# Performance work log

Measured on AMD Instinct MI355X. Metric: run time of the kernel, lower is better.

The kernel has to match this reference:

```python
import jax, jax.numpy as jnp
import numpy as np

N = 50000        # nodes
E = 800000       # edges (avg degree 16)
DIN = 256        # input feature dim
D = 128          # embedding_dim
B = 8            # graphs in batch
ITERS = 2        # num_iterations


def setup_inputs() -> dict:
    key = jax.random.key(0)
    ks = jax.random.split(key, 16)
    w = lambda k, shape: jax.random.normal(k, shape, jnp.float32) * 0.05
    z = lambda n: jnp.zeros((n,), jnp.float32)
    return {
        "nodes": jax.random.normal(ks[0], (N, DIN), jnp.float32),
        "edges": jax.random.randint(ks[1], (2, E), 0, N),
        "batch": jnp.sort(jax.random.randint(ks[2], (N,), 0, B)),
        # initial encoder Linear(DIN, D)
        "W_enc": w(ks[3], (DIN, D)), "b_enc": z(D),
        # parent aggregation MLP: Linear(2D, D) -> ReLU -> Linear(D, D)
        "Wp1": w(ks[4], (2 * D, D)), "bp1": z(D),
        "Wp2": w(ks[5], (D, D)), "bp2": z(D),
        # child aggregation MLP
        "Wc1": w(ks[6], (2 * D, D)), "bc1": z(D),
        "Wc2": w(ks[7], (D, D)), "bc2": z(D),
        # final agg: Linear(3D, 2D) -> ReLU -> Linear(2D, D)
        "Wf1": w(ks[8], (3 * D, 2 * D)), "bf1": z(2 * D),
        "Wf2": w(ks[9], (2 * D, D)), "bf2": z(D),
        # Conv1d(D, 2D, kernel=1) == Linear(D, 2D)
        "Wconv": w(ks[10], (D, 2 * D)), "bconv": z(2 * D),
    }


def _edge_agg(x, idx_i, idx_j, W1, b1, W2, b2, inv_deg):
    # message: mlp(cat(x_i, x_j)); scatter-sum at idx_i; degree-normalize.
    h = jnp.concatenate([x[idx_i], x[idx_j]], axis=1)         # [E, 2D]
    m = jax.nn.relu(h @ W1 + b1) @ W2 + b2                    # [E, D]
    agg = jax.ops.segment_sum(m, idx_i, num_segments=x.shape[0])
    return agg * inv_deg[:, None]


def reference(nodes, edges, batch, W_enc, b_enc, Wp1, bp1, Wp2, bp2,
              Wc1, bc1, Wc2, bc2, Wf1, bf1, Wf2, bf2, Wconv, bconv):
    src, dst = edges[0], edges[1]
    ones_e = jnp.ones((edges.shape[1],), nodes.dtype)
    deg_dst = jax.ops.segment_sum(ones_e, dst, num_segments=N)
    deg_src = jax.ops.segment_sum(ones_e, src, num_segments=N)
    inv_dst = jnp.where(deg_dst > 0, 1.0 / deg_dst, 0.0)
    inv_src = jnp.where(deg_src > 0, 1.0 / deg_src, 0.0)

    x = nodes @ W_enc + b_enc                                  # [N, D]
    for _ in range(ITERS):
        # Parent_Aggregation: x_i = x[dst], x_j = x[src], sum at dst, / in-deg
        fi = _edge_agg(x, dst, src, Wp1, bp1, Wp2, bp2, inv_dst)
        # Child_Aggregation:  x_i = x[src], x_j = x[dst], sum at src, / out-deg
        fo = _edge_agg(x, src, dst, Wc1, bc1, Wc2, bc2, inv_src)
        h = jnp.concatenate([x, fi, fo], axis=1)               # [N, 3D]
        x = x + (jax.nn.relu(h @ Wf1 + bf1) @ Wf2 + bf2)

    y = x @ Wconv + bconv                                      # conv1d k=1 -> [N, 2D]
    gmax = jax.ops.segment_max(y, batch, num_segments=B)       # global_max_pool
    cnt = jax.ops.segment_sum(jnp.ones((N,), y.dtype), batch, num_segments=B)
    gmean = jax.ops.segment_sum(y, batch, num_segments=B) / cnt[:, None]
    return jnp.concatenate([gmax, gmean], axis=1)              # [B, 4D]
```

## Files before the change

kernel.cpp:

```cpp
#include <hip/hip_runtime.h>
#include <hip/hip_bf16.h>
#include <float.h>

typedef __hip_bfloat16 bf16;
typedef short short8 __attribute__((ext_vector_type(8)));
typedef short short4v __attribute__((ext_vector_type(4)));
typedef float f32x4 __attribute__((ext_vector_type(4)));
typedef unsigned short u16;
typedef unsigned char u8;

__device__ __forceinline__ float toF(bf16 v) { return __bfloat162float(v); }
__device__ __forceinline__ float s2f(short s) {
    return __uint_as_float(((unsigned int)(unsigned short)s) << 16);
}
__device__ __forceinline__ short f2s(float f) {
    bf16 h = __float2bfloat16(f);
    return *(short*)&h;
}
__device__ __forceinline__ float rdw(const void* p, int i, int f) {
    return f ? toF(((const bf16*)p)[i]) : ((const float*)p)[i];
}

__global__ void diag_kernel(float* __restrict__ out, float v, int n) {
    int i = blockIdx.x * 256 + threadIdx.x;
    if (i < n) out[i] = v;
}

__global__ void init_kernel(int* __restrict__ deg2, float* __restrict__ cnt_gsum,
                            float* __restrict__ gmax, int* __restrict__ flag, int n2) {
    int i = blockIdx.x * 256 + threadIdx.x;
    if (i < n2) deg2[i] = 0;
    if (i < 8 + 2048) cnt_gsum[i] = 0.f;
    if (i < 2048) gmax[i] = -FLT_MAX;
    if (i == 0) *flag = 1;
}

__global__ void probe_kernel(const unsigned int* __restrict__ w, int nwords,
                             int* __restrict__ flag) {
    int i = blockIdx.x * 256 + threadIdx.x;
    bool bad = false;
    if (i < nwords) {
        float v = __uint_as_float((w[i] & 0xFFFFu) << 16);
        bad = !(v > -1e3f && v < 1e3f);
    }
    if (__any(bad) && (threadIdx.x & 63) == 0) atomicAnd(flag, 0);
}

struct M1 {
    const int* edges; int E;
    int* degd; int* degs; u8* rankd; u8* ranks;
    const int* batch; int Nn; float* cnt;
    const void* wsrc[7]; int woff[7]; bf16* wdst[7];
    int wK[7]; int wNC[7]; int wstart[8];
    const void* bsrc[8]; bf16* bdst[8]; int bn[8];
    const void* b1praw; const void* b1craw; bf16* b1wide;
    const int* flag;
    int sCnt, sSwz, sBias;
};

__global__ void mega1_kernel(M1 a) {
    int b = blockIdx.x, tid = threadIdx.x;
    if (b < a.sCnt) {
        const int* es = a.edges;
        const int* ed = a.edges + a.E;
        int e0 = (b * 256 + tid) * 4;
        if (e0 + 4 <= a.E) {
            int4 s4 = *(const int4*)(es + e0);
            int4 d4 = *(const int4*)(ed + e0);
            uchar4 rs, rd;
            rs.x = (u8)atomicAdd(&a.degs[s4.x], 1);
            rs.y = (u8)atomicAdd(&a.degs[s4.y], 1);
            rs.z = (u8)atomicAdd(&a.degs[s4.z], 1);
            rs.w = (u8)atomicAdd(&a.degs[s4.w], 1);
            rd.x = (u8)atomicAdd(&a.degd[d4.x], 1);
            rd.y = (u8)atomicAdd(&a.degd[d4.y], 1);
            rd.z = (u8)atomicAdd(&a.degd[d4.z], 1);
            rd.w = (u8)atomicAdd(&a.degd[d4.w], 1);
            *(uchar4*)(a.ranks + e0) = rs;
            *(uchar4*)(a.rankd + e0) = rd;
        } else {
            for (int e = e0; e < a.E; ++e) {
                a.ranks[e] = (u8)atomicAdd(&a.degs[es[e]], 1);
                a.rankd[e] = (u8)atomicAdd(&a.degd[ed[e]], 1);
            }
        }
    } else if (b < a.sSwz) {
        __shared__ float loc[8];
        if (tid < 8) loc[tid] = 0.f;
        __syncthreads();
        int i = (b - a.sCnt) * 256 + tid;
        if (i < a.Nn) atomicAdd(&loc[a.batch[i]], 1.0f);
        __syncthreads();
        if (tid < 8 && loc[tid] > 0.f) atomicAdd(&a.cnt[tid], loc[tid]);
    } else if (b < a.sBias) {
        int bb = b - a.sSwz;
        int seg = 0;
#pragma unroll
        for (int t = 1; t < 7; ++t) if (bb >= a.wstart[t]) seg = t;
        int i = (bb - a.wstart[seg]) * 256 + tid;
        int K = a.wK[seg], NC = a.wNC[seg];
        if (i < K * NC) {
            int KF = K >> 5;
            int j = i & 7;
            int ln = (i >> 3) & 63;
            int q = i >> 9;
            int kb = q % KF;
            int t = q / KF;
            int k = kb * 32 + (ln >> 4) * 8 + j;
            int n = t * 16 + (ln & 15);
            int idx = a.woff[seg] + k * NC + n;
            a.wdst[seg][i] = (*a.flag)
                ? ((const bf16*)a.wsrc[seg])[idx]
                : __float2bfloat16(((const float*)a.wsrc[seg])[idx]);
        }
    } else {
        int f = *a.flag;
#pragma unroll
        for (int t = 0; t < 8; ++t)
            for (int i = tid; i < a.bn[t]; i += 256)
                a.bdst[t][i] = f ? ((const bf16*)a.bsrc[t])[i]
                                 : __float2bfloat16(((const float*)a.bsrc[t])[i]);
        for (int i = tid; i < 512; i += 256) {
            float v = 0.f;
            if (i < 128) v = rdw(a.b1praw, i, f);
            else if (i >= 256 && i < 384) v = rdw(a.b1craw, i - 256, f);
            a.b1wide[i] = __float2bfloat16(v);
        }
    }
}

__device__ __forceinline__ void atomicMaxF(float* addr, float val) {
    unsigned int* ua = (unsigned int*)addr;
    unsigned int old = __float_as_uint(*addr);
    while (__uint_as_float(old) < val) {
        unsigned int assumed = old;
        old = atomicCAS(ua, assumed, __float_as_uint(val));
        if (old == assumed) break;
    }
}

template<int K, int NC> struct SB {
    static constexpr int APAD = K + 8;
    static constexpr int CPAD = NC + 8;
    static constexpr int AB = 64 * APAD * 2;
    static constexpr int CB = 64 * CPAD * 2;
    static constexpr int S = AB > CB ? AB : CB;
};

template<int K, int NC, int NSRC, int ADT, bool RELU, bool RES, bool POOL, bool STORE>
__device__ __forceinline__ void gemm_core(int bx,
    const bf16* A0, const bf16* A1, const bf16* A2,
    const bf16* WS, const bf16* bias, bf16* C, int M,
    const int* batch, float* gmax, float* gsum, char* smem) {
    constexpr int KF = K / 32;
    constexpr int NH = NC / 128;
    constexpr int APAD = SB<K, NC>::APAD;
    constexpr int CPAD = SB<K, NC>::CPAD;
    short* sA = (short*)smem;

    int tid = threadIdx.x;
    int m0blk = bx * 64;

    constexpr int C8 = K / 8;
    for (int idx = tid; idx < 64 * C8; idx += 256) {
        int r = idx / C8, c8 = idx % C8;
        int row = m0blk + r; row = row < M ? row : M - 1;
        const bf16* src;
        int off;
        if (NSRC == 1) { src = A0; off = c8 * 8; }
        else {
            int seg = c8 >> 4;
            src = seg == 0 ? A0 : (seg == 1 ? A1 : A2);
            off = (c8 & 15) * 8;
        }
        const size_t rs = (NSRC == 1) ? (size_t)K : (size_t)128;
        if (ADT == 0) {
            *(short8*)(sA + r * APAD + c8 * 8) =
                *(const short8*)((const short*)src + (size_t)row * rs + off);
        } else {
            const float* fp = (const float*)src;
            size_t base = (size_t)row * rs + off;
            float4 v0 = *(const float4*)(fp + base);
            float4 v1 = *(const float4*)(fp + base + 4);
            short8 o;
            o[0] = f2s(v0.x); o[1] = f2s(v0.y); o[2] = f2s(v0.z); o[3] = f2s(v0.w);
            o[4] = f2s(v1.x); o[5] = f2s(v1.y); o[6] = f2s(v1.z); o[7] = f2s(v1.w);
            *(short8*)(sA + r * APAD + c8 * 8) = o;
        }
    }
    __syncthreads();

    int wv = tid >> 6, ln = tid & 63;
    int quad = ln >> 4, ncol = ln & 15;
    int mw = wv * 16;

    short8 a[KF];
#pragma unroll
    for (int kb = 0; kb < KF; ++kb)
        a[kb] = *(const short8*)(sA + (mw + ncol) * APAD + kb * 32 + quad * 8);
    __syncthreads();

    short* sC = (short*)smem;
    const short8* wsp = (const short8*)WS;
#pragma unroll
    for (int h = 0; h < NH; ++h) {
        f32x4 acc[8];
#pragma unroll
        for (int t = 0; t < 8; ++t) acc[t] = (f32x4){0.f, 0.f, 0.f, 0.f};
        short8 bcur[8], bnxt[8];
#pragma unroll
        for (int t = 0; t < 8; ++t)
            bcur[t] = wsp[(size_t)((h * 8 + t) * KF) * 64 + ln];
#pragma unroll
        for (int kb = 0; kb < KF; ++kb) {
            if (kb + 1 < KF) {
#pragma unroll
                for (int t = 0; t < 8; ++t)
                    bnxt[t] = wsp[(size_t)((h * 8 + t) * KF + kb + 1) * 64 + ln];
            }
#pragma unroll
            for (int t = 0; t < 8; ++t)
                acc[t] = __builtin_amdgcn_mfma_f32_16x16x32_bf16(a[kb], bcur[t], acc[t], 0, 0, 0);
#pragma unroll
            for (int t = 0; t < 8; ++t) bcur[t] = bnxt[t];
        }
#pragma unroll
        for (int t = 0; t < 8; ++t) {
            float bv = bias ? toF(bias[h * 128 + t * 16 + ncol]) : 0.f;
#pragma unroll
            for (int r = 0; r < 4; ++r) {
                float v = acc[t][r] + bv;
                if (RELU) v = fmaxf(v, 0.f);
                sC[(mw + quad * 4 + r) * CPAD + h * 128 + t * 16 + ncol] = f2s(v);
            }
        }
    }
    __syncthreads();
    if (!STORE && !POOL) return;

    if (POOL) {
        int* bs = (int*)(smem + SB<K, NC>::S);
        if (tid < 64) {
            int row = m0blk + tid;
            bs[tid] = (row < M) ? batch[row] : -1;
        }
        __syncthreads();
        int cur_b = -1;
        float mx = -FLT_MAX, sm = 0.f;
        for (int r = 0; r < 64; ++r) {
            int b = bs[r];
            if (b < 0) break;
            float v = s2f(sC[r * CPAD + tid]);
            if (b != cur_b) {
                if (cur_b >= 0) {
                    atomicMaxF(&gmax[cur_b * 256 + tid], mx);
                    atomicAdd(&gsum[cur_b * 256 + tid], sm);
                }
                cur_b = b; mx = v; sm = v;
            } else {
                mx = fmaxf(mx, v);
                sm += v;
            }
        }
        if (cur_b >= 0) {
            atomicMaxF(&gmax[cur_b * 256 + tid], mx);
            atomicAdd(&gsum[cur_b * 256 + tid], sm);
        }
    } else {
        constexpr int OC8 = NC / 8;
        for (int idx = tid; idx < 64 * OC8; idx += 256) {
            int r = idx / OC8, c8 = idx % OC8;
            int row = m0blk + r;
            if (row < M) {
                short8 v = *(short8*)(sC + r * CPAD + c8 * 8);
                size_t o = (size_t)row * NC + c8 * 8;
                if (RES) {
                    short8 old = *(const short8*)((const short*)C + o);
#pragma unroll
                    for (int j = 0; j < 8; ++j) v[j] = f2s(s2f(v[j]) + s2f(old[j]));
                }
                *(short8*)((short*)C + o) = v;
            }
        }
    }
}

template<int K, int NC, int NSRC, bool RELU, bool RES, bool POOL>
__global__ __launch_bounds__(256, 2)
void gemm_mfma_kernel(const bf16* A0, const bf16* A1, const bf16* A2,
                      const bf16* WS, const bf16* bias, bf16* C, int M,
                      const int* batch, float* gmax, float* gsum) {
    __shared__ __align__(16) char smem[SB<K, NC>::S + (POOL ? 256 : 0)];
    gemm_core<K, NC, NSRC, 0, RELU, RES, POOL, true>(
        blockIdx.x, A0, A1, A2, WS, bias, C, M, batch, gmax, gsum, smem);
}

__global__ __launch_bounds__(256, 2)
void sei_kernel(const int* __restrict__ edges, int E,
                const u8* __restrict__ rankd, const u8* __restrict__ ranks,
                u16* __restrict__ adjd, u16* __restrict__ adjs, int CAP,
                const void* nodes_raw, const int* flag,
                const bf16* WSenc, const bf16* benc, bf16* x, int M,
                const int* degd, const int* degs,
                float* invd, float* invs,
                const void* w2praw, const void* w2craw, const void* wf1raw,
                const void* b2praw, const void* b2craw,
                bf16* wsf1, bf16* ub, bf16* vb,
                int gsc, int gb) {
    __shared__ __align__(16) char smem[SB<256, 128>::S];
    int b = blockIdx.x, tid = threadIdx.x;
    if (b < 384) {
        int i = b * 256 + tid;
        int j = i & 7;
        int ln2 = (i >> 3) & 63;
        int q = i >> 9;
        int kb = q % 12;
        int t = q / 12;
        int k = kb * 32 + (ln2 >> 4) * 8 + j;
        int n = t * 16 + (ln2 & 15);
        int f = *flag;
        float val;
        if (k < 128) {
            val = rdw(wf1raw, k * 256 + n, f);
        } else {
            const void* w2 = (k < 256) ? w2praw : w2craw;
            int arow = k & 127;
            int base = (k < 256) ? 128 : 256;
            float s = 0.f;
            for (int c = 0; c < 128; ++c)
                s += rdw(w2, arow * 128 + c, f) * rdw(wf1raw, (base + c) * 256 + n, f);
            val = s;
        }
        wsf1[i] = __float2bfloat16(val);
    } else if (b == 384) {
        if (tid < 256) {
            int f = *flag;
            float su = 0.f, sv = 0.f;
            for (int c = 0; c < 128; ++c) {
                su += rdw(b2praw, c, f) * rdw(wf1raw, (128 + c) * 256 + tid, f);
                sv += rdw(b2craw, c, f) * rdw(wf1raw, (256 + c) * 256 + tid, f);
            }
            ub[tid] = __float2bfloat16(su);
            vb[tid] = __float2bfloat16(sv);
        }
    } else if (b < 385 + gsc) {
        int e0 = ((b - 385) * 256 + tid) * 4;
        if (e0 + 4 <= E) {
            int4 s4 = *(const int4*)(edges + e0);
            int4 d4 = *(const int4*)(edges + E + e0);
            uchar4 rs = *(const uchar4*)(ranks + e0);
            uchar4 rd = *(const uchar4*)(rankd + e0);
            if (rs.x < CAP) adjs[s4.x * CAP + rs.x] = (u16)d4.x;
            if (rs.y < CAP) adjs[s4.y * CAP + rs.y] = (u16)d4.y;
            if (rs.z < CAP) adjs[s4.z * CAP + rs.z] = (u16)d4.z;
            if (rs.w < CAP) adjs[s4.w * CAP + rs.w] = (u16)d4.w;
            if (rd.x < CAP) adjd[d4.x * CAP + rd.x] = (u16)s4.x;
            if (rd.y < CAP) adjd[d4.y * CAP + rd.y] = (u16)s4.y;
            if (rd.z < CAP) adjd[d4.z * CAP + rd.z] = (u16)s4.z;
            if (rd.w < CAP) adjd[d4.w * CAP + rd.w] = (u16)s4.w;
        } else {
            for (int e = e0; e < E; ++e) {
                int s_ = edges[e], d_ = edges[E + e];
                if (ranks[e] < CAP) adjs[s_ * CAP + ranks[e]] = (u16)d_;
                if (rankd[e] < CAP) adjd[d_ * CAP + rankd[e]] = (u16)s_;
            }
        }
    } else if (b < 385 + gsc + gb) {
        int bx = b - 385 - gsc;
        if (*flag)
            gemm_core<256, 128, 1, 0, false, false, false, true>(
                bx, (const bf16*)nodes_raw, nullptr, nullptr, WSenc, benc, x, M,
                nullptr, nullptr, nullptr, smem);
        else
            gemm_core<256, 128, 1, 1, false, false, false, true>(
                bx, (const bf16*)nodes_raw, nullptr, nullptr, WSenc, benc, x, M,
                nullptr, nullptr, nullptr, smem);
    } else {
        int i = (b - 385 - gsc - gb) * 256 + tid;
        if (i < M) {
            int dd = degd[i]; invd[i] = dd > 0 ? 1.0f / (float)dd : 0.0f;
            int ds = degs[i]; invs[i] = ds > 0 ? 1.0f / (float)ds : 0.0f;
        }
    }
}

__device__ __forceinline__ void agg_body(int node, int tid,
        const int* __restrict__ deg, const u16* __restrict__ adj, int CAP,
        const float* __restrict__ inv,
        const short* __restrict__ PQ, int stride, bf16* __restrict__ S) {
    int ln = tid & 63;
    int g = ln >> 4, c8 = ln & 15;
    float p[8];
    {
        short8 pv = *(const short8*)(PQ + (size_t)node * stride + c8 * 8);
#pragma unroll
        for (int r = 0; r < 8; ++r) p[r] = s2f(pv[r]);
    }
    float a[8] = {0.f, 0.f, 0.f, 0.f, 0.f, 0.f, 0.f, 0.f};
    int d = deg[node]; d = d < CAP ? d : CAP;
    float invv = inv[node];
    const u16* ap = adj + (size_t)node * CAP;
    const short* Qb = PQ + 128 + c8 * 8;
    int k = g;
    for (; k + 28 < d; k += 32) {
        int j0 = ap[k],      j1 = ap[k + 4],  j2 = ap[k + 8],  j3 = ap[k + 12];
        int j4 = ap[k + 16], j5 = ap[k + 20], j6 = ap[k + 24], j7 = ap[k + 28];
        short8 q0 = *(const short8*)(Qb + (size_t)j0 * stride);
        short8 q1 = *(const short8*)(Qb + (size_t)j1 * stride);
        short8 q2 = *(const short8*)(Qb + (size_t)j2 * stride);
        short8 q3 = *(const short8*)(Qb + (size_t)j3 * stride);
        short8 q4 = *(const short8*)(Qb + (size_t)j4 * stride);
        short8 q5 = *(const short8*)(Qb + (size_t)j5 * stride);
        short8 q6 = *(const short8*)(Qb + (size_t)j6 * stride);
        short8 q7 = *(const short8*)(Qb + (size_t)j7 * stride);
#pragma unroll
        for (int r = 0; r < 8; ++r)
            a[r] += fmaxf(p[r] + s2f(q0[r]), 0.f) + fmaxf(p[r] + s2f(q1[r]), 0.f)
                  + fmaxf(p[r] + s2f(q2[r]), 0.f) + fmaxf(p[r] + s2f(q3[r]), 0.f)
                  + fmaxf(p[r] + s2f(q4[r]), 0.f) + fmaxf(p[r] + s2f(q5[r]), 0.f)
                  + fmaxf(p[r] + s2f(q6[r]), 0.f) + fmaxf(p[r] + s2f(q7[r]), 0.f);
    }
    for (; k + 12 < d; k += 16) {
        int j0 = ap[k], j1 = ap[k + 4], j2 = ap[k + 8], j3 = ap[k + 12];
        short8 q0 = *(const short8*)(Qb + (size_t)j0 * stride);
        short8 q1 = *(const short8*)(Qb + (size_t)j1 * stride);
        short8 q2 = *(const short8*)(Qb + (size_t)j2 * stride);
        short8 q3 = *(const short8*)(Qb + (size_t)j3 * stride);
#pragma unroll
        for (int r = 0; r < 8; ++r)
            a[r] += fmaxf(p[r] + s2f(q0[r]), 0.f) + fmaxf(p[r] + s2f(q1[r]), 0.f)
                  + fmaxf(p[r] + s2f(q2[r]), 0.f) + fmaxf(p[r] + s2f(q3[r]), 0.f);
    }
    for (; k < d; k += 4) {
        int j = ap[k];
        short8 q = *(const short8*)(Qb + (size_t)j * stride);
#pragma unroll
        for (int r = 0; r < 8; ++r) a[r] += fmaxf(p[r] + s2f(q[r]), 0.f);
    }
#pragma unroll
    for (int r = 0; r < 8; ++r) {
        a[r] += __shfl_xor(a[r], 16);
        a[r] += __shfl_xor(a[r], 32);
    }
    if (g == 0) {
        short8 o;
#pragma unroll
        for (int r = 0; r < 8; ++r) o[r] = f2s(a[r] * invv);
        *(short8*)((short*)S + (size_t)node * 128 + c8 * 8) = o;
    }
}

__global__ __launch_bounds__(256, 4)
void agg_kernel(const int* deg, const u16* adj, int CAP,
                const float* inv, const bf16* PQ, int stride,
                bf16* S, int M) {
    int node = blockIdx.x * 4 + (threadIdx.x >> 6);
    if (node >= M) return;
    agg_body(node, threadIdx.x, deg, adj, CAP, inv, (const short*)PQ, stride, S);
}

__global__ __launch_bounds__(256, 4)
void agg2_kernel(const int* degd, const u16* adjd, const float* invd,
                 const int* degs, const u16* adjs, const float* invs,
                 int CAP, const bf16* T, bf16* Sd, bf16* Ss, int M, int ga) {
    int b = blockIdx.x, wv = threadIdx.x >> 6;
    if (b < ga) {
        int node = b * 4 + wv;
        if (node < M)
            agg_body(node, threadIdx.x, degd, adjd, CAP, invd, (const short*)T, 512, Sd);
    } else {
        int node = (b - ga) * 4 + wv;
        if (node < M)
            agg_body(node, threadIdx.x, degs, adjs, CAP, invs, (const short*)T + 256, 512, Ss);
    }
}

template<bool FINAL>
__global__ __launch_bounds__(256, 2)
void mega_mlp_kernel(const bf16* __restrict__ x, const bf16* Sd, const bf16* Ss,
                     const int* __restrict__ degd, const int* __restrict__ degs,
                     const bf16* __restrict__ ub, const bf16* __restrict__ vb,
                     const bf16* WSf1, const bf16* bf1_,
                     const bf16* WSf2, const bf16* bf2_,
                     bf16* xio, int M,
                     const bf16* WSconv, const bf16* bconv,
                     const int* batch, float* gmax, float* gsum) {
    __shared__ __align__(16) char smem[52224 + 256];
    constexpr int RB = 17408;
    short* sm = (short*)smem;
    int tid = threadIdx.x;
    int m0blk = blockIdx.x * 64;

#pragma unroll
    for (int reg = 0; reg < 3; ++reg) {
        const short* sp = reg == 0 ? (const short*)x
                        : (reg == 1 ? (const short*)Sd : (const short*)Ss);
        for (int idx = tid; idx < 64 * 16; idx += 256) {
            int r = idx >> 4, c8 = idx & 15;
            int row = m0blk + r; row = row < M ? row : M - 1;
            *(short8*)(sm + reg * (RB / 2) + r * 136 + c8 * 8) =
                *(const short8*)(sp + (size_t)row * 128 + c8 * 8);
        }
    }
    __syncthreads();

    int wv = tid >> 6, ln = tid & 63;
    int quad = ln >> 4, ncol = ln & 15;
    int mw = wv * 16;

    short8 a1[12];
#pragma unroll
    for (int kb = 0; kb < 12; ++kb) {
        const short* sb = sm + (kb >> 2) * (RB / 2);
        a1[kb] = *(const short8*)(sb + (mw + ncol) * 136 + (kb & 3) * 32 + quad * 8);
    }
    __syncthreads();

    bool md[4], ms[4];
#pragma unroll
    for (int r = 0; r < 4; ++r) {
        int orow = m0blk + mw + quad * 4 + r; orow = orow < M ? orow : M - 1;
        md[r] = degd[orow] > 0;
        ms[r] = degs[orow] > 0;
    }

    short* sH = sm + RB / 2;
    const short8* w1 = (const short8*)WSf1;
#pragma unroll
    for (int h = 0; h < 2; ++h) {
        f32x4 acc[8];
#pragma unroll
        for (int t = 0; t < 8; ++t) acc[t] = (f32x4){0.f, 0.f, 0.f, 0.f};
        short8 bcur[8], bnxt[8];
#pragma unroll
        for (int t = 0; t < 8; ++t)
            bcur[t] = w1[(size_t)((h * 8 + t) * 12) * 64 + ln];
#pragma unroll
        for (int kb = 0; kb < 12; ++kb) {
            if (kb + 1 < 12) {
#pragma unroll
                for (int t = 0; t < 8; ++t)
                    bnxt[t] = w1[(size_t)((h * 8 + t) * 12 + kb + 1) * 64 + ln];
            }
#pragma unroll
            for (int t = 0; t < 8; ++t)
                acc[t] = __builtin_amdgcn_mfma_f32_16x16x32_bf16(a1[kb], bcur[t], acc[t], 0, 0, 0);
#pragma unroll
            for (int t = 0; t < 8; ++t) bcur[t] = bnxt[t];
        }
#pragma unroll
        for (int t = 0; t < 8; ++t) {
            int col = h * 128 + t * 16 + ncol;
            float bv = toF(bf1_[col]);
            float uu = toF(ub[col]);
            float vv = toF(vb[col]);
#pragma unroll
            for (int r = 0; r < 4; ++r) {
                float v = acc[t][r] + bv + (md[r] ? uu : 0.f) + (ms[r] ? vv : 0.f);
                sH[(mw + quad * 4 + r) * 264 + col] = f2s(fmaxf(v, 0.f));
            }
        }
    }
    __syncthreads();

    short8 a2[8];
#pragma unroll
    for (int kb = 0; kb < 8; ++kb)
        a2[kb] = *(const short8*)(sH + (mw + ncol) * 264 + kb * 32 + quad * 8);
    __syncthreads();

    f32x4 acc2[8];
#pragma unroll
    for (int t = 0; t < 8; ++t) acc2[t] = (f32x4){0.f, 0.f, 0.f, 0.f};
    const short8* w2 = (const short8*)WSf2;
    {
        short8 bcur[8], bnxt[8];
#pragma unroll
        for (int t = 0; t < 8; ++t) bcur[t] = w2[(size_t)(t * 8) * 64 + ln];
#pragma unroll
        for (int kb = 0; kb < 8; ++kb) {
            if (kb + 1 < 8) {
#pragma unroll
                for (int t = 0; t < 8; ++t)
                    bnxt[t] = w2[(size_t)(t * 8 + kb + 1) * 64 + ln];
            }
#pragma unroll
            for (int t = 0; t < 8; ++t)
                acc2[t] = __builtin_amdgcn_mfma_f32_16x16x32_bf16(a2[kb], bcur[t], acc2[t], 0, 0, 0);
#pragma unroll
            for (int t = 0; t < 8; ++t) bcur[t] = bnxt[t];
        }
    }
    short* sC2 = sm + RB / 2;
#pragma unroll
    for (int t = 0; t < 8; ++t) {
        float bv = toF(bf2_[t * 16 + ncol]);
#pragma unroll
        for (int r = 0; r < 4; ++r)
            sC2[(mw + quad * 4 + r) * 136 + t * 16 + ncol] = f2s(acc2[t][r] + bv);
    }
    __syncthreads();

    for (int idx = tid; idx < 64 * 16; idx += 256) {
        int r = idx >> 4, c8 = idx & 15;
        short8 v = *(short8*)(sC2 + r * 136 + c8 * 8);
        short8 old = *(const short8*)(sm + r * 136 + c8 * 8);
#pragma unroll
        for (int j = 0; j < 8; ++j) v[j] = f2s(s2f(v[j]) + s2f(old[j]));
        if (FINAL) {
            *(short8*)(sC2 + r * 136 + c8 * 8) = v;
        } else {
            int row = m0blk + r;
            if (row < M) *(short8*)((short*)xio + (size_t)row * 128 + c8 * 8) = v;
        }
    }
    if (!FINAL) return;
    __syncthreads();

    short8 a3[4];
#pragma unroll
    for (int kb = 0; kb < 4; ++kb)
        a3[kb] = *(const short8*)(sC2 + (mw + ncol) * 136 + kb * 32 + quad * 8);
    __syncthreads();

    short* sCc = sm;
    const short8* wc = (const short8*)WSconv;
#pragma unroll
    for (int h = 0; h < 2; ++h) {
        f32x4 acc[8];
#pragma unroll
        for (int t = 0; t < 8; ++t) acc[t] = (f32x4){0.f, 0.f, 0.f, 0.f};
        short8 bcur[8], bnxt[8];
#pragma unroll
        for (int t = 0; t < 8; ++t)
            bcur[t] = wc[(size_t)((h * 8 + t) * 4) * 64 + ln];
#pragma unroll
        for (int kb = 0; kb < 4; ++kb) {
            if (kb + 1 < 4) {
#pragma unroll
                for (int t = 0; t < 8; ++t)
                    bnxt[t] = wc[(size_t)((h * 8 + t) * 4 + kb + 1) * 64 + ln];
            }
#pragma unroll
            for (int t = 0; t < 8; ++t)
                acc[t] = __builtin_amdgcn_mfma_f32_16x16x32_bf16(a3[kb], bcur[t], acc[t], 0, 0, 0);
#pragma unroll
            for (int t = 0; t < 8; ++t) bcur[t] = bnxt[t];
        }
#pragma unroll
        for (int t = 0; t < 8; ++t) {
            float bv = toF(bconv[h * 128 + t * 16 + ncol]);
#pragma unroll
            for (int r = 0; r < 4; ++r)
                sCc[(mw + quad * 4 + r) * 264 + h * 128 + t * 16 + ncol] =
                    f2s(acc[t][r] + bv);
        }
    }
    __syncthreads();

    int* bs = (int*)(smem + 52224);
    if (tid < 64) {
        int row = m0blk + tid;
        bs[tid] = (row < M) ? batch[row] : -1;
    }
    __syncthreads();
    int cur_b = -1;
    float mx = -FLT_MAX, sum_ = 0.f;
    for (int r = 0; r < 64; ++r) {
        int b = bs[r];
        if (b < 0) break;
        float v = s2f(sCc[r * 264 + tid]);
        if (b != cur_b) {
            if (cur_b >= 0) {
                atomicMaxF(&gmax[cur_b * 256 + tid], mx);
                atomicAdd(&gsum[cur_b * 256 + tid], sum_);
            }
            cur_b = b; mx = v; sum_ = v;
        } else {
            mx = fmaxf(mx, v);
            sum_ += v;
        }
    }
    if (cur_b >= 0) {
        atomicMaxF(&gmax[cur_b * 256 + tid], mx);
        atomicAdd(&gsum[cur_b * 256 + tid], sum_);
    }
}

__global__ void out_kernel(const float* __restrict__ gmax, const float* __restrict__ gsum,
                           const float* __restrict__ cnt, const int* __restrict__ flag,
                           void* __restrict__ out) {
    int i = blockIdx.x * 256 + threadIdx.x;
    if (i < 8 * 512) {
        int b = i >> 9, c = i & 511;
        float v = (c < 256) ? gmax[b * 256 + c] : gsum[b * 256 + (c - 256)] / cnt[b];
        int f = *flag;
        if (!(v == v)) v = 1000.f + 100.f * (float)f;
        if (f) ((bf16*)out)[i] = __float2bfloat16(v);
        else   ((float*)out)[i] = v;
    }
}

extern "C" void kernel_launch(void* const* d_in, const int* in_sizes, int n_in,
                              void* d_out, int out_size, void* d_ws, size_t ws_size,
                              hipStream_t stream) {
    const int* edges = (const int*)d_in[1];
    const int* batch = (const int*)d_in[2];

    const int N_ = in_sizes[2];
    const int E_ = in_sizes[1] / 2;
    const size_t ND = (size_t)N_ * 128;

    char* p = (char*)d_ws;
    bf16* x  = (bf16*)p;      p += ND * 2;
    bf16* Sd = (bf16*)p;      p += ND * 2;
    bf16* Ss = (bf16*)p;      p += ND * 2;
    bf16* bias[8];
    for (int t = 0; t < 8; ++t) { bias[t] = (bf16*)p; p += 512 * 2; }
    bf16* ub      = (bf16*)p; p += 256 * 2;
    bf16* vb      = (bf16*)p; p += 256 * 2;
    bf16* b1wide  = (bf16*)p; p += 512 * 2;
    bf16* WSenc   = (bf16*)p; p += 256 * 128 * 2;
    bf16* WSpqall = (bf16*)p; p += 4 * 128 * 128 * 2;
    bf16* WSf1    = (bf16*)p; p += 384 * 256 * 2;
    bf16* WSf2    = (bf16*)p; p += 256 * 128 * 2;
    bf16* WSconv  = (bf16*)p; p += 128 * 256 * 2;
    int* degd    = (int*)p;   p += (size_t)N_ * 4;
    int* degs    = (int*)p;   p += (size_t)N_ * 4;
    float* invd  = (float*)p; p += (size_t)N_ * 4;
    float* invs  = (float*)p; p += (size_t)N_ * 4;
    float* cnt   = (float*)p; p += 8 * 4;
    float* gsum  = (float*)p; p += 2048 * 4;
    float* gmax  = (float*)p; p += 2048 * 4;
    int* flag    = (int*)p;   p += 64;
    u8* rankd    = (u8*)p;    p += ((size_t)E_ + 15) & ~(size_t)15;
    u8* ranks    = (u8*)p;    p += ((size_t)E_ + 15) & ~(size_t)15;

    size_t used = (size_t)(p - (char*)d_ws);
    size_t rem = ws_size > used ? ws_size - used : 0;
    int CAP = 0, wide = 0;
    if (N_ < 65536) {
        if      (rem >= (size_t)2 * N_ * 64 * 2 + (size_t)N_ * 512 * 2) { CAP = 64; wide = 1; }
        else if (rem >= (size_t)2 * N_ * 64 * 2 + (size_t)N_ * 256 * 2) { CAP = 64; wide = 0; }
        else if (rem >= (size_t)2 * N_ * 48 * 2 + (size_t)N_ * 256 * 2) { CAP = 48; wide = 0; }
    }
    if (!CAP) {
        diag_kernel<<<(out_size + 255) / 256, 256, 0, stream>>>((float*)d_out, (float)(ws_size >> 20), out_size);
        return;
    }
    u16* adjd = (u16*)p;      p += (size_t)N_ * CAP * 2;
    u16* adjs = (u16*)p;      p += (size_t)N_ * CAP * 2;
    bf16* T   = (bf16*)p;

    int gN  = (N_ + 255) / 256;
    int gE4 = (E_ + 1023) / 1024;
    int gb  = (N_ + 63) / 64;
    int ga  = (N_ + 3) / 4;

    init_kernel<<<(2 * N_ + 255) / 256, 256, 0, stream>>>(degd, cnt, gmax, flag, 2 * N_);
    probe_kernel<<<8, 256, 0, stream>>>((const unsigned int*)d_in[3], 2048, flag);

    M1 a;
    a.edges = edges; a.E = E_;
    a.degd = degd; a.degs = degs; a.rankd = rankd; a.ranks = ranks;
    a.batch = batch; a.Nn = N_; a.cnt = cnt;
    a.b1praw = d_in[6]; a.b1craw = d_in[10]; a.b1wide = b1wide;
    {
        const int bidx[8] = {4, 6, 8, 10, 12, 14, 16, 18};
        for (int t = 0; t < 8; ++t) {
            a.bsrc[t] = d_in[bidx[t]];
            a.bdst[t] = bias[t];
            a.bn[t] = in_sizes[bidx[t]];
        }
        const void* wraw[7] = {d_in[3], d_in[5], d_in[5], d_in[9], d_in[9],
                               d_in[15], d_in[17]};
        int woff[7]  = {0, 0, 128 * 128, 0, 128 * 128, 0, 0};
        bf16* wdst[7] = {WSenc, WSpqall, WSpqall + 16384, WSpqall + 32768,
                         WSpqall + 49152, WSf2, WSconv};
        int wK[7]  = {256, 128, 128, 128, 128, 256, 128};
        int wNC[7] = {128, 128, 128, 128, 128, 128, 256};
        int wb_ = 0;
        for (int t = 0; t < 7; ++t) {
            a.wsrc[t] = wraw[t]; a.woff[t] = woff[t]; a.wdst[t] = wdst[t];
            a.wK[t] = wK[t]; a.wNC[t] = wNC[t];
            a.wstart[t] = wb_;
            wb_ += (wK[t] * wNC[t] + 255) / 256;
        }
        a.wstart[7] = wb_;
        a.flag = flag;
        a.sCnt  = gE4;
        a.sSwz  = a.sCnt + gN;
        a.sBias = a.sSwz + wb_;
        mega1_kernel<<<a.sBias + 1, 256, 0, stream>>>(a);
    }

    sei_kernel<<<385 + gE4 + gb + gN, 256, 0, stream>>>(
        edges, E_, rankd, ranks, adjd, adjs, CAP,
        d_in[0], flag, WSenc, bias[0], x, N_,
        degd, degs, invd, invs,
        d_in[7], d_in[11], d_in[13], d_in[8], d_in[12],
        WSf1, ub, vb, gE4, gb);

    for (int it = 0; it < 2; ++it) {
        if (wide) {
            gemm_mfma_kernel<128, 512, 1, false, false, false><<<gb, 256, 0, stream>>>(
                x, nullptr, nullptr, WSpqall, b1wide, T, N_, nullptr, nullptr, nullptr);
            agg2_kernel<<<2 * ga, 256, 0, stream>>>(degd, adjd, invd, degs, adjs, invs,
                                                    CAP, T, Sd, Ss, N_, ga);
        } else {
            gemm_mfma_kernel<128, 256, 1, false, false, false><<<gb, 256, 0, stream>>>(
                x, nullptr, nullptr, WSpqall, b1wide, T, N_, nullptr, nullptr, nullptr);
            agg_kernel<<<ga, 256, 0, stream>>>(degd, adjd, CAP, invd, T, 256, Sd, N_);
            gemm_mfma_kernel<128, 256, 1, false, false, false><<<gb, 256, 0, stream>>>(
                x, nullptr, nullptr, WSpqall + 32768, b1wide + 256, T, N_, nullptr, nullptr, nullptr);
            agg_kernel<<<ga, 256, 0, stream>>>(degs, adjs, CAP, invs, T, 256, Ss, N_);
        }
        if (it == 0)
            mega_mlp_kernel<false><<<gb, 256, 0, stream>>>(
                x, Sd, Ss, degd, degs, ub, vb,
                WSf1, bias[5], WSf2, bias[6], x, N_,
                WSconv, bias[7], batch, gmax, gsum);
        else
            mega_mlp_kernel<true><<<gb, 256, 0, stream>>>(
                x, Sd, Ss, degd, degs, ub, vb,
                WSf1, bias[5], WSf2, bias[6], x, N_,
                WSconv, bias[7], batch, gmax, gsum);
    }

    out_kernel<<<16, 256, 0, stream>>>(gmax, gsum, cnt, flag, d_out);
}
```

Before: 632.3 us.

## Fuse next-iteration PQ projection into MLP kernel and use per-wave LDS tiles

The generic gemm kernel for the per-node edge-MLP first-layer projection is replaced by a dedicated pq_kernel. Each wave keeps its own 16-row LDS tile, so there are no block-wide barriers and occupancy can rise. In the wide path, the first-iteration mega_mlp kernel also computes the second iteration's 512-wide projection from the freshly updated x held in LDS. This removes one kernel launch and the re-read of x. mega_mlp now loads its A operands directly from global memory instead of staging them through shared memory, and smaller per-block LDS allows 4 blocks per CU. The tradeoff is more register pressure and uncoalesced direct row loads.

After: 600.4 us. 5.0% less time.

```diff
diff --git a/kernel.cpp b/kernel.cpp
--- a/kernel.cpp
+++ b/kernel.cpp
@@ -283,16 +283,6 @@
             }
         }
     }
-}
-
-template<int K, int NC, int NSRC, bool RELU, bool RES, bool POOL>
-__global__ __launch_bounds__(256, 2)
-void gemm_mfma_kernel(const bf16* A0, const bf16* A1, const bf16* A2,
-                      const bf16* WS, const bf16* bias, bf16* C, int M,
-                      const int* batch, float* gmax, float* gsum) {
-    __shared__ __align__(16) char smem[SB<K, NC>::S + (POOL ? 256 : 0)];
-    gemm_core<K, NC, NSRC, 0, RELU, RES, POOL, true>(
-        blockIdx.x, A0, A1, A2, WS, bias, C, M, batch, gmax, gsum, smem);
 }
 
 __global__ __launch_bounds__(256, 2)
@@ -384,6 +374,67 @@
     }
 }
 
+template<int NC>
+__global__ __launch_bounds__(256, 4)
+void pq_kernel(const bf16* __restrict__ x, const bf16* __restrict__ WSpq,
+               const bf16* __restrict__ b1w, bf16* __restrict__ T, int M) {
+    __shared__ __align__(16) short sb[4][16 * 136];
+    int tid = threadIdx.x;
+    int wv = tid >> 6, ln = tid & 63;
+    int quad = ln >> 4, ncol = ln & 15;
+    int mw = wv * 16;
+    int m0 = blockIdx.x * 64;
+    short* B = &sb[wv][0];
+
+    int arow = m0 + mw + ncol; arow = arow < M ? arow : M - 1;
+    short8 a[4];
+#pragma unroll
+    for (int kb = 0; kb < 4; ++kb)
+        a[kb] = *(const short8*)((const short*)x + (size_t)arow * 128 + kb * 32 + quad * 8);
+
+    const short8* wsp = (const short8*)WSpq;
+    constexpr int NH = NC / 128;
+#pragma unroll
+    for (int h = 0; h < NH; ++h) {
+        f32x4 acc[8];
+#pragma unroll
+        for (int t = 0; t < 8; ++t) acc[t] = (f32x4){0.f, 0.f, 0.f, 0.f};
+        short8 bcur[8], bnxt[8];
+#pragma unroll
+        for (int t = 0; t < 8; ++t)
+            bcur[t] = wsp[(size_t)((h * 8 + t) * 4) * 64 + ln];
+#pragma unroll
+        for (int kb = 0; kb < 4; ++kb) {
+            if (kb + 1 < 4) {
+#pragma unroll
+                for (int t = 0; t < 8; ++t)
+                    bnxt[t] = wsp[(size_t)((h * 8 + t) * 4 + kb + 1) * 64 + ln];
+            }
+#pragma unroll
+            for (int t = 0; t < 8; ++t)
+                acc[t] = __builtin_amdgcn_mfma_f32_16x16x32_bf16(a[kb], bcur[t], acc[t], 0, 0, 0);
+#pragma unroll
+            for (int t = 0; t < 8; ++t) bcur[t] = bnxt[t];
+        }
+#pragma unroll
+        for (int t = 0; t < 8; ++t) {
+            float bv = toF(b1w[h * 128 + t * 16 + ncol]);
+#pragma unroll
+            for (int r = 0; r < 4; ++r)
+                B[(quad * 4 + r) * 136 + t * 16 + ncol] = f2s(acc[t][r] + bv);
+        }
+#pragma unroll
+        for (int it2 = 0; it2 < 4; ++it2) {
+            int idx = it2 * 64 + ln;
+            int r = idx >> 4, c8 = idx & 15;
+            int row = m0 + mw + r;
+            if (row < M)
+                *(short8*)((short*)T + (size_t)row * NC + h * 128 + c8 * 8) =
+                    *(short8*)(B + r * 136 + c8 * 8);
+        }
+    }
+}
+
 __device__ __forceinline__ void agg_body(int node, int tid,
         const int* __restrict__ deg, const u16* __restrict__ adj, int CAP,
         const float* __restrict__ inv,
@@ -476,55 +527,40 @@
 }
 
 template<bool FINAL>
-__global__ __launch_bounds__(256, 2)
+__global__ __launch_bounds__(256, 4)
 void mega_mlp_kernel(const bf16* __restrict__ x, const bf16* Sd, const bf16* Ss,
                      const int* __restrict__ degd, const int* __restrict__ degs,
                      const bf16* __restrict__ ub, const bf16* __restrict__ vb,
                      const bf16* WSf1, const bf16* bf1_,
                      const bf16* WSf2, const bf16* bf2_,
-                     bf16* xio, int M,
+                     bf16* xio, bf16* Tw, const bf16* WSpq, const bf16* b1w, int M,
                      const bf16* WSconv, const bf16* bconv,
                      const int* batch, float* gmax, float* gsum) {
-    __shared__ __align__(16) char smem[52224 + 256];
-    constexpr int RB = 17408;
-    short* sm = (short*)smem;
+    __shared__ __align__(16) short sH[4][16 * 264];
+    __shared__ int bs[64];
     int tid = threadIdx.x;
-    int m0blk = blockIdx.x * 64;
-
-#pragma unroll
-    for (int reg = 0; reg < 3; ++reg) {
-        const short* sp = reg == 0 ? (const short*)x
-                        : (reg == 1 ? (const short*)Sd : (const short*)Ss);
-        for (int idx = tid; idx < 64 * 16; idx += 256) {
-            int r = idx >> 4, c8 = idx & 15;
-            int row = m0blk + r; row = row < M ? row : M - 1;
-            *(short8*)(sm + reg * (RB / 2) + r * 136 + c8 * 8) =
-                *(const short8*)(sp + (size_t)row * 128 + c8 * 8);
-        }
-    }
-    __syncthreads();
-
     int wv = tid >> 6, ln = tid & 63;
     int quad = ln >> 4, ncol = ln & 15;
     int mw = wv * 16;
-
+    int m0 = blockIdx.x * 64;
+    short* H = &sH[wv][0];
+
+    int arow = m0 + mw + ncol; arow = arow < M ? arow : M - 1;
     short8 a1[12];
 #pragma unroll
-    for (int kb = 0; kb < 12; ++kb) {
-        const short* sb = sm + (kb >> 2) * (RB / 2);
-        a1[kb] = *(const short8*)(sb + (mw + ncol) * 136 + (kb & 3) * 32 + quad * 8);
-    }
-    __syncthreads();
-
+    for (int kb = 0; kb < 4; ++kb) {
+        a1[kb]     = *(const short8*)((const short*)x  + (size_t)arow * 128 + kb * 32 + quad * 8);
+        a1[4 + kb] = *(const short8*)((const short*)Sd + (size_t)arow * 128 + kb * 32 + quad * 8);
+        a1[8 + kb] = *(const short8*)((const short*)Ss + (size_t)arow * 128 + kb * 32 + quad * 8);
+    }
     bool md[4], ms[4];
 #pragma unroll
     for (int r = 0; r < 4; ++r) {
-        int orow = m0blk + mw + quad * 4 + r; orow = orow < M ? orow : M - 1;
+        int orow = m0 + mw + quad * 4 + r; orow = orow < M ? orow : M - 1;
         md[r] = degd[orow] > 0;
         ms[r] = degs[orow] > 0;
     }
 
-    short* sH = sm + RB / 2;
     const short8* w1 = (const short8*)WSf1;
 #pragma unroll
     for (int h = 0; h < 2; ++h) {
@@ -557,18 +593,15 @@
 #pragma unroll
             for (int r = 0; r < 4; ++r) {
                 float v = acc[t][r] + bv + (md[r] ? uu : 0.f) + (ms[r] ? vv : 0.f);
-                sH[(mw + quad * 4 + r) * 264 + col] = f2s(fmaxf(v, 0.f));
-            }
-        }
-    }
-    __syncthreads();
+                H[(quad * 4 + r) * 264 + col] = f2s(fmaxf(v, 0.f));
+            }
+        }
+    }
 
     short8 a2[8];
 #pragma unroll
     for (int kb = 0; kb < 8; ++kb)
-        a2[kb] = *(const short8*)(sH + (mw + ncol) * 264 + kb * 32 + quad * 8);
-    __syncthreads();
-
+        a2[kb] = *(const short8*)(H + ncol * 264 + kb * 32 + quad * 8);
     f32x4 acc2[8];
 #pragma unroll
     for (int t = 0; t < 8; ++t) acc2[t] = (f32x4){0.f, 0.f, 0.f, 0.f};
@@ -591,39 +624,83 @@
             for (int t = 0; t < 8; ++t) bcur[t] = bnxt[t];
         }
     }
-    short* sC2 = sm + RB / 2;
 #pragma unroll
     for (int t = 0; t < 8; ++t) {
         float bv = toF(bf2_[t * 16 + ncol]);
 #pragma unroll
         for (int r = 0; r < 4; ++r)
-            sC2[(mw + quad * 4 + r) * 136 + t * 16 + ncol] = f2s(acc2[t][r] + bv);
-    }
-    __syncthreads();
-
-    for (int idx = tid; idx < 64 * 16; idx += 256) {
+            H[(quad * 4 + r) * 136 + t * 16 + ncol] = f2s(acc2[t][r] + bv);
+    }
+
+#pragma unroll
+    for (int it2 = 0; it2 < 4; ++it2) {
+        int idx = it2 * 64 + ln;
         int r = idx >> 4, c8 = idx & 15;
-        short8 v = *(short8*)(sC2 + r * 136 + c8 * 8);
-        short8 old = *(const short8*)(sm + r * 136 + c8 * 8);
+        int row = m0 + mw + r;
+        int rowc = row < M ? row : M - 1;
+        short8 v = *(short8*)(H + r * 136 + c8 * 8);
+        short8 old = *(const short8*)((const short*)x + (size_t)rowc * 128 + c8 * 8);
 #pragma unroll
         for (int j = 0; j < 8; ++j) v[j] = f2s(s2f(v[j]) + s2f(old[j]));
-        if (FINAL) {
-            *(short8*)(sC2 + r * 136 + c8 * 8) = v;
-        } else {
-            int row = m0blk + r;
-            if (row < M) *(short8*)((short*)xio + (size_t)row * 128 + c8 * 8) = v;
-        }
-    }
-    if (!FINAL) return;
-    __syncthreads();
+        *(short8*)(H + r * 136 + c8 * 8) = v;
+        if (!FINAL && row < M)
+            *(short8*)((short*)xio + (size_t)row * 128 + c8 * 8) = v;
+    }
+
+    if (!FINAL) {
+        if (Tw) {
+            short8 a3[4];
+#pragma unroll
+            for (int kb = 0; kb < 4; ++kb)
+                a3[kb] = *(const short8*)(H + ncol * 136 + kb * 32 + quad * 8);
+            const short8* wpq = (const short8*)WSpq;
+#pragma unroll
+            for (int h = 0; h < 4; ++h) {
+                f32x4 acc[8];
+#pragma unroll
+                for (int t = 0; t < 8; ++t) acc[t] = (f32x4){0.f, 0.f, 0.f, 0.f};
+                short8 bcur[8], bnxt[8];
+#pragma unroll
+                for (int t = 0; t < 8; ++t)
+                    bcur[t] = wpq[(size_t)((h * 8 + t) * 4) * 64 + ln];
+#pragma unroll
+                for (int kb = 0; kb < 4; ++kb) {
+                    if (kb + 1 < 4) {
+#pragma unroll
+                        for (int t = 0; t < 8; ++t)
+                            bnxt[t] = wpq[(size_t)((h * 8 + t) * 4 + kb + 1) * 64 + ln];
+                    }
+#pragma unroll
+                    for (int t = 0; t < 8; ++t)
+                        acc[t] = __builtin_amdgcn_mfma_f32_16x16x32_bf16(a3[kb], bcur[t], acc[t], 0, 0, 0);
+#pragma unroll
+                    for (int t = 0; t < 8; ++t) bcur[t] = bnxt[t];
+                }
+#pragma unroll
+                for (int t = 0; t < 8; ++t) {
+                    float bv = toF(b1w[h * 128 + t * 16 + ncol]);
+#pragma unroll
+                    for (int r = 0; r < 4; ++r)
+                        H[(quad * 4 + r) * 136 + t * 16 + ncol] = f2s(acc[t][r] + bv);
+                }
+#pragma unroll
+                for (int it2 = 0; it2 < 4; ++it2) {
+                    int idx = it2 * 64 + ln;
+                    int r = idx >> 4, c8 = idx & 15;
+                    int row = m0 + mw + r;
+                    if (row < M)
+                        *(short8*)((short*)Tw + (size_t)row * 512 + h * 128 + c8 * 8) =
+                            *(short8*)(H + r * 136 + c8 * 8);
+                }
+            }
+        }
+        return;
+    }
 
     short8 a3[4];
 #pragma unroll
     for (int kb = 0; kb < 4; ++kb)
-        a3[kb] = *(const short8*)(sC2 + (mw + ncol) * 136 + kb * 32 + quad * 8);
-    __syncthreads();
-
-    short* sCc = sm;
+        a3[kb] = *(const short8*)(H + ncol * 136 + kb * 32 + quad * 8);
     const short8* wc = (const short8*)WSconv;
 #pragma unroll
     for (int h = 0; h < 2; ++h) {
@@ -652,24 +729,22 @@
             float bv = toF(bconv[h * 128 + t * 16 + ncol]);
 #pragma unroll
             for (int r = 0; r < 4; ++r)
-                sCc[(mw + quad * 4 + r) * 264 + h * 128 + t * 16 + ncol] =
-                    f2s(acc[t][r] + bv);
-        }
+                H[(quad * 4 + r) * 264 + h * 128 + t * 16 + ncol] = f2s(acc[t][r] + bv);
+        }
+    }
+    if (tid < 64) {
+        int row = m0 + tid;
+        bs[tid] = (row < M) ? batch[row] : -1;
     }
     __syncthreads();
 
-    int* bs = (int*)(smem + 52224);
-    if (tid < 64) {
-        int row = m0blk + tid;
-        bs[tid] = (row < M) ? batch[row] : -1;
-    }
-    __syncthreads();
+    const short* flat = &sH[0][0];
     int cur_b = -1;
     float mx = -FLT_MAX, sum_ = 0.f;
     for (int r = 0; r < 64; ++r) {
         int b = bs[r];
         if (b < 0) break;
-        float v = s2f(sCc[r * 264 + tid]);
+        float v = s2f(flat[r * 264 + tid]);
         if (b != cur_b) {
             if (cur_b >= 0) {
                 atomicMaxF(&gmax[cur_b * 256 + tid], mx);
@@ -801,30 +876,33 @@
         d_in[7], d_in[11], d_in[13], d_in[8], d_in[12],
         WSf1, ub, vb, gE4, gb);
 
-    for (int it = 0; it < 2; ++it) {
-        if (wide) {
-            gemm_mfma_kernel<128, 512, 1, false, false, false><<<gb, 256, 0, stream>>>(
-                x, nullptr, nullptr, WSpqall, b1wide, T, N_, nullptr, nullptr, nullptr);
-            agg2_kernel<<<2 * ga, 256, 0, stream>>>(degd, adjd, invd, degs, adjs, invs,
-                                                    CAP, T, Sd, Ss, N_, ga);
-        } else {
-            gemm_mfma_kernel<128, 256, 1, false, false, false><<<gb, 256, 0, stream>>>(
-                x, nullptr, nullptr, WSpqall, b1wide, T, N_, nullptr, nullptr, nullptr);
+    if (wide) {
+        pq_kernel<512><<<gb, 256, 0, stream>>>(x, WSpqall, b1wide, T, N_);
+        agg2_kernel<<<2 * ga, 256, 0, stream>>>(degd, adjd, invd, degs, adjs, invs,
+                                                CAP, T, Sd, Ss, N_, ga);
+        mega_mlp_kernel<false><<<gb, 256, 0, stream>>>(
+            x, Sd, Ss, degd, degs, ub, vb, WSf1, bias[5], WSf2, bias[6],
+            x, T, WSpqall, b1wide, N_, WSconv, bias[7], batch, gmax, gsum);
+        agg2_kernel<<<2 * ga, 256, 0, stream>>>(degd, adjd, invd, degs, adjs, invs,
+                                                CAP, T, Sd, Ss, N_, ga);
+        mega_mlp_kernel<true><<<gb, 256, 0, stream>>>(
+            x, Sd, Ss, degd, degs, ub, vb, WSf1, bias[5], WSf2, bias[6],
+            x, nullptr, nullptr, nullptr, N_, WSconv, bias[7], batch, gmax, gsum);
+    } else {
+        for (int it = 0; it < 2; ++it) {
+            pq_kernel<256><<<gb, 256, 0, stream>>>(x, WSpqall, b1wide, T, N_);
             agg_kernel<<<ga, 256, 0, stream>>>(degd, adjd, CAP, invd, T, 256, Sd, N_);
-            gemm_mfma_kernel<128, 256, 1, false, false, false><<<gb, 256, 0, stream>>>(
-                x, nullptr, nullptr, WSpqall + 32768, b1wide + 256, T, N_, nullptr, nullptr, nullptr);
+            pq_kernel<256><<<gb, 256, 0, stream>>>(x, WSpqall + 32768, b1wide + 256, T, N_);
             agg_kernel<<<ga, 256, 0, stream>>>(degs, adjs, CAP, invs, T, 256, Ss, N_);
-        }
-        if (it == 0)
-            mega_mlp_kernel<false><<<gb, 256, 0, stream>>>(
-                x, Sd, Ss, degd, degs, ub, vb,
-                WSf1, bias[5], WSf2, bias[6], x, N_,
-                WSconv, bias[7], batch, gmax, gsum);
-        else
-            mega_mlp_kernel<true><<<gb, 256, 0, stream>>>(
-                x, Sd, Ss, degd, degs, ub, vb,
-                WSf1, bias[5], WSf2, bias[6], x, N_,
-                WSconv, bias[7], batch, gmax, gsum);
+            if (it == 0)
+                mega_mlp_kernel<false><<<gb, 256, 0, stream>>>(
+                    x, Sd, Ss, degd, degs, ub, vb, WSf1, bias[5], WSf2, bias[6],
+                    x, nullptr, nullptr, nullptr, N_, WSconv, bias[7], batch, gmax, gsum);
+            else
+                mega_mlp_kernel<true><<<gb, 256, 0, stream>>>(
+                    x, Sd, Ss, degd, degs, ub, vb, WSf1, bias[5], WSf2, bias[6],
+                    x, nullptr, nullptr, nullptr, N_, WSconv, bias[7], batch, gmax, gsum);
+        }
     }
 
     out_kernel<<<16, 256, 0, stream>>>(gmax, gsum, cnt, flag, d_out);
```
